# Optimization experiments

Measured on AMD Instinct MI355X. Metric: run time of the kernel, lower is better.

Reference implementation:

```python
import jax, jax.numpy as jnp
import numpy as np

N, B, E, H = 2048, 4, 256, 8
DH = E // H


def setup_inputs() -> dict:
    key = jax.random.key(0)
    ks = jax.random.split(key, 10)
    s = 1.0 / np.sqrt(E)
    f = lambda k, sh, sc=1.0: (jax.random.normal(k, sh, jnp.float32) * sc)
    return {
        "x": f(ks[0], (N, B, E)),
        "query_pos": f(ks[1], (N, B, E), 0.1),
        "receiver_val_res": f(ks[2], (N, B, E), 0.1),
        "sender_val_res": f(ks[3], (N, B, E), 0.1),
        "Wq": f(ks[4], (E, E), s), "bq": jnp.zeros((E,), jnp.float32),
        "Wk": f(ks[5], (E, E), s), "bk": jnp.zeros((E,), jnp.float32),
        "Wr": f(ks[6], (E, E), s), "br": jnp.zeros((E,), jnp.float32),
        "Ws": f(ks[7], (E, E), s), "bs_v": jnp.zeros((E,), jnp.float32),
        "Wo": f(ks[8], (E, E), s), "bo": jnp.zeros((E,), jnp.float32),
    }


def reference(x, query_pos, receiver_val_res, sender_val_res,
              Wq, bq, Wk, bk, Wr, br, Ws, bs_v, Wo, bo):
    # wrapper: key = query = x; key_pos = query_pos (same shape); residual = x
    q_in = x + query_pos  # [N,B,E]
    scale = 1.0 / np.sqrt(DH)
    q = (q_in @ Wq + bq).reshape(N, B, H, DH)
    k = (q_in @ Wk + bk).reshape(N, B, H, DH)
    # TIE edge-value decomposition: per-particle receiver/sender value tokens,
    # with accumulated cross-layer value residuals added.
    vr = q_in @ Wr + br + receiver_val_res  # [N,B,E]
    vs = q_in @ Ws + bs_v + sender_val_res  # [N,B,E]
    scores = jnp.einsum('nbhd,mbhd->bhnm', q, k) * scale  # [B,H,N,N]
    attn = jax.nn.softmax(scores, axis=-1)
    # out_i = sum_j a_ij (vr_i + vs_j) = vr_i + sum_j a_ij vs_j  (rows sum to 1)
    ctx = jnp.einsum('bhnm,mbhd->nbhd', attn, vs.reshape(N, B, H, DH))
    ctx = ctx + vr.reshape(N, B, H, DH)
    out = ctx.reshape(N, B, E) @ Wo + bo
    return (x + out, vr, vs)
```

## Files before the change

### kernel.cpp

```cpp
#include <hip/hip_runtime.h>
#include <hip/hip_bf16.h>

#define NTOK 2048
#define BATCH 4
#define EMB 256
#define NH 8
#define DHD 32
#define MROWS (NTOK*BATCH)
#define NBE (MROWS*EMB)

typedef __attribute__((ext_vector_type(8))) __bf16 bf16x8;
typedef __attribute__((ext_vector_type(4))) float f32x4;
typedef __attribute__((ext_vector_type(8))) unsigned short ushort8;
typedef __attribute__((ext_vector_type(4))) unsigned int uint4v;

__device__ __forceinline__ unsigned short f2bf(float f){
  unsigned int u = __builtin_bit_cast(unsigned int, f);
  u += 0x7fffu + ((u >> 16) & 1u);
  return (unsigned short)(u >> 16);
}
__device__ __forceinline__ float fexp2(float x){
#if __has_builtin(__builtin_amdgcn_exp2f)
  return __builtin_amdgcn_exp2f(x);
#else
  return exp2f(x);
#endif
}

#define QSC (0.17677669529663687f * 1.4426950408889634f)


__global__ __launch_bounds__(256) void k_add(const float* __restrict__ x,
                                             const float* __restrict__ qp,
                                             unsigned short* __restrict__ qpk){
  int t = blockIdx.x * 256 + threadIdx.x;
  int ppos = t * 8;
  int tile = ppos >> 12;
  int rem  = ppos & 4095;
  int kc   = rem >> 9;
  int row  = (rem >> 5) & 15;
  int kk   = rem & 31;
  int src  = (tile*16 + row)*256 + kc*32 + kk;
  f32x4 a0 = *(const f32x4*)(x + src);
  f32x4 a1 = *(const f32x4*)(x + src + 4);
  f32x4 b0 = *(const f32x4*)(qp + src);
  f32x4 b1 = *(const f32x4*)(qp + src + 4);
  ushort8 o;
#pragma unroll
  for (int j = 0; j < 4; ++j){
    o[j]   = f2bf(a0[j] + b0[j]);
    o[j+4] = f2bf(a1[j] + b1[j]);
  }
  *(ushort8*)(qpk + ppos) = o;
}

__global__ __launch_bounds__(256) void k_transW(const float* __restrict__ s0,
                                                const float* __restrict__ s1,
                                                const float* __restrict__ s2,
                                                const float* __restrict__ s3,
                                                const float* __restrict__ s4,
                                                unsigned short* __restrict__ wt){
  const float* srcs[5] = {s0, s1, s2, s3, s4};
  __shared__ float lds[64][65];
  int wi = blockIdx.z;
  int k0 = blockIdx.x * 64;
  int n0 = blockIdx.y * 64;
  int tid = threadIdx.x;
  const float* src = srcs[wi];
#pragma unroll
  for (int p = 0; p < 4; ++p){
    int r = p*16 + (tid>>4);
    int c = (tid&15)*4;
    f32x4 v = *(const f32x4*)(src + (k0+r)*256 + n0 + c);
#pragma unroll
    for (int j = 0; j < 4; ++j) lds[r][c+j] = v[j];
  }
  __syncthreads();
#pragma unroll
  for (int p = 0; p < 4; ++p){
    int nr = p*16 + (tid>>4);
    int kc = (tid&15)*4;
    unsigned long long pk = 0;
#pragma unroll
    for (int j = 0; j < 4; ++j)
      pk |= ((unsigned long long)f2bf(lds[kc+j][nr])) << (16*j);
    int n_g = n0 + nr, k_g = k0 + kc;
    int pos = (n_g>>4)*4096 + (k_g>>5)*512 + (n_g&15)*32 + (k_g&31);
    *(unsigned long long*)(wt + wi*65536 + pos) = pk;
  }
}

__global__ __launch_bounds__(256) void k_proj(const unsigned short* __restrict__ qpk,
                                              const unsigned short* __restrict__ wt,
                                              const float* __restrict__ bq,
                                              const float* __restrict__ bk,
                                              const float* __restrict__ br,
                                              const float* __restrict__ bs,
                                              const float* __restrict__ recv,
                                              const float* __restrict__ send,
                                              unsigned short* __restrict__ qbuf,
                                              unsigned short* __restrict__ kpk,
                                              unsigned short* __restrict__ vpk,
                                              float* __restrict__ vrout,
                                              float* __restrict__ vsout){
  int m0 = blockIdx.x * 64;
  int gc = blockIdx.y * 64;
  int widx = gc >> 8;
  int c0 = gc & 255;
  int tid = threadIdx.x;
  int w = tid >> 6, lane = tid & 63;
  int lr = lane & 15, lg = lane >> 4;

  __shared__ __align__(16) float shmemF[64*68];

  const unsigned short* apk = qpk + (m0/16 + w)*4096 + lr*32 + lg*8;
  const unsigned short* bpk = wt + widx*65536 + (c0/16)*4096 + lr*32 + lg*8;

  f32x4 acc[4];
#pragma unroll
  for (int f = 0; f < 4; ++f) acc[f] = (f32x4){0.f, 0.f, 0.f, 0.f};

#pragma unroll
  for (int k0 = 0; k0 < 256; k0 += 32){
    int kb = (k0 >> 5) * 512;
    bf16x8 af = *(const bf16x8*)(apk + kb);
#pragma unroll
    for (int f = 0; f < 4; ++f){
      bf16x8 bfrag = *(const bf16x8*)(bpk + f*4096 + kb);
      acc[f] = __builtin_amdgcn_mfma_f32_16x16x32_bf16(af, bfrag, acc[f], 0, 0, 0);
    }
  }

  const float* bias = (widx == 0) ? bq : (widx == 1) ? bk : (widx == 2) ? br : bs;

  if (widx <= 1){
    unsigned short (*st)[16][72] = (unsigned short(*)[16][72])shmemF;
#pragma unroll
    for (int f = 0; f < 4; ++f){
#pragma unroll
      for (int i = 0; i < 4; ++i){
        int c = c0 + f*16 + lr;
        float v = acc[f][i] + bias[c];
        st[w][lg*4+i][f*16+lr] = f2bf(widx == 0 ? v * QSC : v);
      }
    }
    if (widx == 0){
      int r = lane >> 2, co = (lane & 3) * 16;
      ushort8 a0 = *(ushort8*)&st[w][r][co];
      ushort8 a1 = *(ushort8*)&st[w][r][co + 8];
      unsigned short* dst = qbuf + (m0 + w*16 + r) * 256 + c0 + co;
      *(ushort8*)dst = a0;
      *(ushort8*)(dst + 8) = a1;
    } else {
      int cid = lane >> 3, s = lane & 7;
      int bb = cid >> 1, hr = cid & 1;
      int toko = s >> 1, dp = (s & 1) * 16;
      ushort8 a0 = *(ushort8*)&st[w][toko*4 + bb][hr*32 + dp];
      ushort8 a1 = *(ushort8*)&st[w][toko*4 + bb][hr*32 + dp + 8];
      int h  = (c0 >> 5) + hr;
      int n0 = (m0 + w*16) >> 2;
      int t0 = n0 & 63;
      int p0 = (((t0>>5)&1)<<4) + (((t0>>2)&1)<<5) + (((t0>>3)&3)<<2);
      unsigned short* dst = kpk + (bb*8 + h)*65536 + ((n0 & ~63) + p0 + toko)*32 + dp;
      *(ushort8*)dst = a0;
      *(ushort8*)(dst + 8) = a1;
    }
  } else {
    float (*ldsF)[68] = (float(*)[68])shmemF;
#pragma unroll
    for (int f = 0; f < 4; ++f){
#pragma unroll
      for (int i = 0; i < 4; ++i){
        ldsF[w*16 + lg*4 + i][f*16 + lr] = acc[f][i] + bias[c0 + f*16 + lr];
      }
    }
    __syncthreads();
    const float* gsrc = (widx == 2) ? recv : send;
    float* gdst = (widx == 2) ? vrout : vsout;
#pragma unroll
    for (int k = 0; k < 4; ++k){
      int chunk = k*256 + tid;
      int r = chunk >> 4;
      int cc = (chunk & 15) * 4;
      int idx = (m0 + r)*256 + c0 + cc;
      f32x4 v = *(const f32x4*)&ldsF[r][cc];
      f32x4 g = *(const f32x4*)(gsrc + idx);
#pragma unroll
      for (int j = 0; j < 4; ++j) v[j] += g[j];
      *(f32x4*)(gdst + idx) = v;
    }
    if (widx == 3){
      int bid = blockIdx.x;
      int tile = bid >> 1;
      int cid = tid >> 5;
      int bb = cid >> 1, hr = cid & 1;
      int d = tid & 31;
      int h0 = c0 >> 5;
      int bh = bb*8 + h0 + hr;
      unsigned short* tbase = vpk + (bh*64 + tile)*1024 + d*8;
#pragma unroll
      for (int s8 = 0; s8 < 2; ++s8){
        int sub = 2*(bid & 1) + s8;
        ushort8 o;
#pragma unroll
        for (int j = 0; j < 8; ++j)
          o[j] = f2bf(ldsF[(s8*8 + j)*4 + bb][hr*32 + d] + gsrc[(m0 + (s8*8+j)*4 + bb)*256 + c0 + hr*32 + d]);
        *(ushort8*)(tbase + sub*256) = o;
      }
    }
  }
}

__global__ __launch_bounds__(256) void k_attn(const unsigned short* __restrict__ qbuf,
                                              const unsigned short* __restrict__ kpk,
                                              const unsigned short* __restrict__ vpk,
                                              const float* __restrict__ vrbuf,
                                              unsigned short* __restrict__ ctx){
  int bid = blockIdx.x;
  int bh  = (bid & 7) + ((bid >> 8) << 3);
  int qt0 = ((bid >> 3) & 31) * 64;
  int b = bh >> 3, h = bh & 7;
  int tid = threadIdx.x;
  int w = tid >> 6, lane = tid & 63;
  int wq = w & 1;
  int wk = w >> 1;
  int lr = lane & 15, lg = lane >> 4;
  int lg4 = lg * 4;

  __shared__ float part[2][2][64][9];

  int qbase = qt0 + wq*32;
  bf16x8 qfA = *(const bf16x8*)(qbuf + ((qbase + lr)*BATCH + b)*EMB + h*DHD + lg*8);
  bf16x8 qfB = *(const bf16x8*)(qbuf + ((qbase + 16 + lr)*BATCH + b)*EMB + h*DHD + lg*8);

  const unsigned short* kbase = kpk + bh*65536 + wk*(1024*32) + lr*32 + lg*8;
  const unsigned short* vbase = vpk + bh*65536 + wk*(32*1024) + lg*256 + lr*8;

  f32x4 accA0 = (f32x4){0.f,0.f,0.f,0.f};
  f32x4 accA1 = (f32x4){0.f,0.f,0.f,0.f};
  f32x4 accB0 = (f32x4){0.f,0.f,0.f,0.f};
  f32x4 accB1 = (f32x4){0.f,0.f,0.f,0.f};
  float lsumA = 0.f, lsumB = 0.f;

  bf16x8 kA[4], vA[4], kB[4], vB[4];

  auto loadfr = [&](int kv0, bf16x8* kf, bf16x8* vf){
#pragma unroll
    for (int j = 0; j < 4; ++j)
      kf[j] = *(const bf16x8*)(kbase + (kv0 + j*16)*32);
#pragma unroll
    for (int c = 0; c < 2; ++c)
#pragma unroll
      for (int dh = 0; dh < 2; ++dh)
        vf[c*2+dh] = *(const bf16x8*)(vbase + ((kv0>>5) + c)*1024 + dh*128);
  };

  auto tile_compute = [&](const bf16x8* kf, const bf16x8* vf){
    f32x4 z = (f32x4){0.f,0.f,0.f,0.f};
    f32x4 sA[4], sB[4];
#pragma unroll
    for (int j = 0; j < 4; ++j){
      sA[j] = __builtin_amdgcn_mfma_f32_16x16x32_bf16(kf[j], qfA, z, 0, 0, 0);
      sB[j] = __builtin_amdgcn_mfma_f32_16x16x32_bf16(kf[j], qfB, z, 0, 0, 0);
    }

    float pA[4][4], pB[4][4];
    float psA = 0.f, psB = 0.f;
#pragma unroll
    for (int j = 0; j < 4; ++j){
#pragma unroll
      for (int i = 0; i < 4; ++i){
        pA[j][i] = fexp2(sA[j][i]);
        pB[j][i] = fexp2(sB[j][i]);
      }
      psA += (pA[j][0] + pA[j][1]) + (pA[j][2] + pA[j][3]);
      psB += (pB[j][0] + pB[j][1]) + (pB[j][2] + pB[j][3]);
    }
    lsumA += psA;
    lsumB += psB;

#pragma unroll
    for (int c = 0; c < 2; ++c){
      uint4v dA, dB;
      dA[0] = __builtin_amdgcn_perm(__builtin_bit_cast(unsigned int, pA[c][1]),
                                    __builtin_bit_cast(unsigned int, pA[c][0]), 0x07060302u);
      dA[1] = __builtin_amdgcn_perm(__builtin_bit_cast(unsigned int, pA[c][3]),
                                    __builtin_bit_cast(unsigned int, pA[c][2]), 0x07060302u);
      dA[2] = __builtin_amdgcn_perm(__builtin_bit_cast(unsigned int, pA[c+2][1]),
                                    __builtin_bit_cast(unsigned int, pA[c+2][0]), 0x07060302u);
      dA[3] = __builtin_amdgcn_perm(__builtin_bit_cast(unsigned int, pA[c+2][3]),
                                    __builtin_bit_cast(unsigned int, pA[c+2][2]), 0x07060302u);
      bf16x8 pfA = __builtin_bit_cast(bf16x8, dA);
      accA0 = __builtin_amdgcn_mfma_f32_16x16x32_bf16(pfA, vf[c*2+0], accA0, 0, 0, 0);
      accA1 = __builtin_amdgcn_mfma_f32_16x16x32_bf16(pfA, vf[c*2+1], accA1, 0, 0, 0);
      dB[0] = __builtin_amdgcn_perm(__builtin_bit_cast(unsigned int, pB[c][1]),
                                    __builtin_bit_cast(unsigned int, pB[c][0]), 0x07060302u);
      dB[1] = __builtin_amdgcn_perm(__builtin_bit_cast(unsigned int, pB[c][3]),
                                    __builtin_bit_cast(unsigned int, pB[c][2]), 0x07060302u);
      dB[2] = __builtin_amdgcn_perm(__builtin_bit_cast(unsigned int, pB[c+2][1]),
                                    __builtin_bit_cast(unsigned int, pB[c+2][0]), 0x07060302u);
      dB[3] = __builtin_amdgcn_perm(__builtin_bit_cast(unsigned int, pB[c+2][3]),
                                    __builtin_bit_cast(unsigned int, pB[c+2][2]), 0x07060302u);
      bf16x8 pfB = __builtin_bit_cast(bf16x8, dB);
      accB0 = __builtin_amdgcn_mfma_f32_16x16x32_bf16(pfB, vf[c*2+0], accB0, 0, 0, 0);
      accB1 = __builtin_amdgcn_mfma_f32_16x16x32_bf16(pfB, vf[c*2+1], accB1, 0, 0, 0);
    }
  };

  loadfr(0, kA, vA);
  for (int t = 0; t < 16; t += 2){
    loadfr((t+1)*64, kB, vB);
    tile_compute(kA, vA);
    if (t + 2 < 16) loadfr((t+2)*64, kA, vA);
    tile_compute(kB, vB);
  }

  lsumA += __shfl_xor(lsumA, 16);
  lsumA += __shfl_xor(lsumA, 32);
  lsumB += __shfl_xor(lsumB, 16);
  lsumB += __shfl_xor(lsumB, 32);

  if (wk == 1){
#pragma unroll
    for (int i = 0; i < 4; ++i){
      part[wq][0][lane][i]   = accA0[i];
      part[wq][0][lane][4+i] = accA1[i];
      part[wq][1][lane][i]   = accB0[i];
      part[wq][1][lane][4+i] = accB1[i];
    }
    part[wq][0][lane][8] = lsumA;
    part[wq][1][lane][8] = lsumB;
  }
  __syncthreads();
  if (wk == 0){
#pragma unroll
    for (int i = 0; i < 4; ++i){
      accA0[i] += part[wq][0][lane][i];
      accA1[i] += part[wq][0][lane][4+i];
      accB0[i] += part[wq][1][lane][i];
      accB1[i] += part[wq][1][lane][4+i];
    }
    lsumA += part[wq][0][lane][8];
    lsumB += part[wq][1][lane][8];
    float invA = 1.0f / lsumA;
    float invB = 1.0f / lsumB;
#pragma unroll
    for (int i = 0; i < 4; ++i){
      float vinvA = __shfl(invA, lg4 + i);
      float vinvB = __shfl(invB, lg4 + i);
      int qA = qbase + lg4 + i;
      int idxA = (qA*4 + b)*256 + h*DHD + lr;
      int posA = (qA>>2)*4096 + h*512 + (4*(qA&3)+b)*32 + lr;
      ctx[posA]      = f2bf(accA0[i] * vinvA + vrbuf[idxA]);
      ctx[posA + 16] = f2bf(accA1[i] * vinvA + vrbuf[idxA + 16]);
      int qB = qbase + 16 + lg4 + i;
      int idxB = (qB*4 + b)*256 + h*DHD + lr;
      int posB = (qB>>2)*4096 + h*512 + (4*(qB&3)+b)*32 + lr;
      ctx[posB]      = f2bf(accB0[i] * vinvB + vrbuf[idxB]);
      ctx[posB + 16] = f2bf(accB1[i] * vinvB + vrbuf[idxB + 16]);
    }
  }
}

__global__ __launch_bounds__(256) void k_out(const unsigned short* __restrict__ ctx,
                                             const unsigned short* __restrict__ wt,
                                             const float* __restrict__ bo,
                                             const float* __restrict__ x,
                                             float* __restrict__ out0){
  int m0 = blockIdx.x * 64;
  int c0 = blockIdx.y * 64;
  int tid = threadIdx.x;
  int w = tid >> 6, lane = tid & 63;
  int lr = lane & 15, lg = lane >> 4;

  __shared__ __align__(16) float ldsF[64][68];

  const unsigned short* apk = ctx + (m0/16 + w)*4096 + lr*32 + lg*8;
  const unsigned short* bpk = wt + 4*65536 + (c0/16)*4096 + lr*32 + lg*8;

  f32x4 acc[4];
#pragma unroll
  for (int f = 0; f < 4; ++f) acc[f] = (f32x4){0.f, 0.f, 0.f, 0.f};

#pragma unroll
  for (int k0 = 0; k0 < 256; k0 += 32){
    int kb = (k0 >> 5) * 512;
    bf16x8 af = *(const bf16x8*)(apk + kb);
#pragma unroll
    for (int f = 0; f < 4; ++f){
      bf16x8 bfrag = *(const bf16x8*)(bpk + f*4096 + kb);
      acc[f] = __builtin_amdgcn_mfma_f32_16x16x32_bf16(af, bfrag, acc[f], 0, 0, 0);
    }
  }

#pragma unroll
  for (int f = 0; f < 4; ++f){
#pragma unroll
    for (int i = 0; i < 4; ++i){
      ldsF[w*16 + lg*4 + i][f*16 + lr] = acc[f][i] + bo[c0 + f*16 + lr];
    }
  }
  __syncthreads();
#pragma unroll
  for (int k = 0; k < 4; ++k){
    int chunk = k*256 + tid;
    int r = chunk >> 4;
    int cc = (chunk & 15) * 4;
    int idx = (m0 + r)*256 + c0 + cc;
    f32x4 v = *(const f32x4*)&ldsF[r][cc];
    f32x4 g = *(const f32x4*)(x + idx);
#pragma unroll
    for (int j = 0; j < 4; ++j) v[j] += g[j];
    *(f32x4*)(out0 + idx) = v;
  }
}

extern "C" void kernel_launch(void* const* d_in, const int* in_sizes, int n_in,
                              void* d_out, int out_size, void* d_ws, size_t ws_size,
                              hipStream_t stream){
  const float* x    = (const float*)d_in[0];
  const float* qp   = (const float*)d_in[1];
  const float* recv = (const float*)d_in[2];
  const float* send = (const float*)d_in[3];
  const float* Wq   = (const float*)d_in[4];
  const float* bq   = (const float*)d_in[5];
  const float* Wk   = (const float*)d_in[6];
  const float* bk   = (const float*)d_in[7];
  const float* Wr   = (const float*)d_in[8];
  const float* br   = (const float*)d_in[9];
  const float* Wsv  = (const float*)d_in[10];
  const float* bsv  = (const float*)d_in[11];
  const float* Wo   = (const float*)d_in[12];
  const float* bo   = (const float*)d_in[13];

  float* out0  = (float*)d_out;
  float* vrout = out0 + NBE;
  float* vsout = out0 + 2*NBE;

  unsigned short* ws   = (unsigned short*)d_ws;
  unsigned short* qin  = ws;
  unsigned short* qbuf = ws + NBE;
  unsigned short* kpk  = ws + 2*NBE;
  unsigned short* vpk  = ws + 3*NBE;
  unsigned short* wt   = ws + 4*NBE;

  hipLaunchKernelGGL(k_add, dim3(NBE/8/256), dim3(256), 0, stream, x, qp, qin);
  hipLaunchKernelGGL(k_transW, dim3(4, 4, 5), dim3(256), 0, stream, Wq, Wk, Wr, Wsv, Wo, wt);
  hipLaunchKernelGGL(k_proj, dim3(128, 16), dim3(256), 0, stream,
                     qin, wt, bq, bk, br, bsv, recv, send, qbuf, kpk, vpk, vrout, vsout);
  hipLaunchKernelGGL(k_attn, dim3(1024), dim3(256), 0, stream,
                     qbuf, kpk, vpk, vrout, qin );
  hipLaunchKernelGGL(k_out, dim3(128, 4), dim3(256), 0, stream,
                     qin , wt, bo, x, out0);
}
```

Measured before the change: 78.84 us.

## Split attention KV range across four waves per 32-query block

Each attention block now handles 32 queries instead of 64, and its four waves each cover a quarter of the key/value sequence rather than two waves per half. The grid doubles to 2048 blocks, and partial accumulators from three waves are reduced through shared memory into wave 0. Launch bounds now request higher occupancy (6 blocks per CU). The aim is more parallelism and a shorter serial KV loop per wave. The cost is that K/V traffic per query is duplicated across more blocks and the shared-memory reduction gets larger.

```diff
diff --git a/kernel.cpp b/kernel.cpp
--- a/kernel.cpp
+++ b/kernel.cpp
@@ -211,30 +211,27 @@
   }
 }
 
-__global__ __launch_bounds__(256) void k_attn(const unsigned short* __restrict__ qbuf,
-                                              const unsigned short* __restrict__ kpk,
-                                              const unsigned short* __restrict__ vpk,
-                                              const float* __restrict__ vrbuf,
-                                              unsigned short* __restrict__ ctx){
+__global__ __launch_bounds__(256, 6) void k_attn(const unsigned short* __restrict__ qbuf,
+                                                 const unsigned short* __restrict__ kpk,
+                                                 const unsigned short* __restrict__ vpk,
+                                                 const float* __restrict__ vrbuf,
+                                                 unsigned short* __restrict__ ctx){
   int bid = blockIdx.x;
-  int bh  = (bid & 7) + ((bid >> 8) << 3);
-  int qt0 = ((bid >> 3) & 31) * 64;
+  int bh  = (bid & 7) + ((bid >> 9) << 3);
+  int qbase = ((bid >> 3) & 63) * 32;
   int b = bh >> 3, h = bh & 7;
   int tid = threadIdx.x;
   int w = tid >> 6, lane = tid & 63;
-  int wq = w & 1;
-  int wk = w >> 1;
   int lr = lane & 15, lg = lane >> 4;
   int lg4 = lg * 4;
 
-  __shared__ float part[2][2][64][9];
-
-  int qbase = qt0 + wq*32;
+  __shared__ float part[3][2][64][9];
+
   bf16x8 qfA = *(const bf16x8*)(qbuf + ((qbase + lr)*BATCH + b)*EMB + h*DHD + lg*8);
   bf16x8 qfB = *(const bf16x8*)(qbuf + ((qbase + 16 + lr)*BATCH + b)*EMB + h*DHD + lg*8);
 
-  const unsigned short* kbase = kpk + bh*65536 + wk*(1024*32) + lr*32 + lg*8;
-  const unsigned short* vbase = vpk + bh*65536 + wk*(32*1024) + lg*256 + lr*8;
+  const unsigned short* kbase = kpk + bh*65536 + w*16384 + lr*32 + lg*8;
+  const unsigned short* vbase = vpk + bh*65536 + w*16384 + lg*256 + lr*8;
 
   f32x4 accA0 = (f32x4){0.f,0.f,0.f,0.f};
   f32x4 accA1 = (f32x4){0.f,0.f,0.f,0.f};
@@ -308,10 +305,10 @@
   };
 
   loadfr(0, kA, vA);
-  for (int t = 0; t < 16; t += 2){
+  for (int t = 0; t < 8; t += 2){
     loadfr((t+1)*64, kB, vB);
     tile_compute(kA, vA);
-    if (t + 2 < 16) loadfr((t+2)*64, kA, vA);
+    if (t + 2 < 8) loadfr((t+2)*64, kA, vA);
     tile_compute(kB, vB);
   }
 
@@ -320,28 +317,31 @@
   lsumB += __shfl_xor(lsumB, 16);
   lsumB += __shfl_xor(lsumB, 32);
 
-  if (wk == 1){
+  if (w > 0){
 #pragma unroll
     for (int i = 0; i < 4; ++i){
-      part[wq][0][lane][i]   = accA0[i];
-      part[wq][0][lane][4+i] = accA1[i];
-      part[wq][1][lane][i]   = accB0[i];
-      part[wq][1][lane][4+i] = accB1[i];
-    }
-    part[wq][0][lane][8] = lsumA;
-    part[wq][1][lane][8] = lsumB;
+      part[w-1][0][lane][i]   = accA0[i];
+      part[w-1][0][lane][4+i] = accA1[i];
+      part[w-1][1][lane][i]   = accB0[i];
+      part[w-1][1][lane][4+i] = accB1[i];
+    }
+    part[w-1][0][lane][8] = lsumA;
+    part[w-1][1][lane][8] = lsumB;
   }
   __syncthreads();
-  if (wk == 0){
-#pragma unroll
-    for (int i = 0; i < 4; ++i){
-      accA0[i] += part[wq][0][lane][i];
-      accA1[i] += part[wq][0][lane][4+i];
-      accB0[i] += part[wq][1][lane][i];
-      accB1[i] += part[wq][1][lane][4+i];
-    }
-    lsumA += part[wq][0][lane][8];
-    lsumB += part[wq][1][lane][8];
+  if (w == 0){
+#pragma unroll
+    for (int ww = 0; ww < 3; ++ww){
+#pragma unroll
+      for (int i = 0; i < 4; ++i){
+        accA0[i] += part[ww][0][lane][i];
+        accA1[i] += part[ww][0][lane][4+i];
+        accB0[i] += part[ww][1][lane][i];
+        accB1[i] += part[ww][1][lane][4+i];
+      }
+      lsumA += part[ww][0][lane][8];
+      lsumB += part[ww][1][lane][8];
+    }
     float invA = 1.0f / lsumA;
     float invB = 1.0f / lsumB;
 #pragma unroll
@@ -448,7 +448,7 @@
   hipLaunchKernelGGL(k_transW, dim3(4, 4, 5), dim3(256), 0, stream, Wq, Wk, Wr, Wsv, Wo, wt);
   hipLaunchKernelGGL(k_proj, dim3(128, 16), dim3(256), 0, stream,
                      qin, wt, bq, bk, br, bsv, recv, send, qbuf, kpk, vpk, vrout, vsout);
-  hipLaunchKernelGGL(k_attn, dim3(1024), dim3(256), 0, stream,
+  hipLaunchKernelGGL(k_attn, dim3(2048), dim3(256), 0, stream,
                      qbuf, kpk, vpk, vrout, qin );
   hipLaunchKernelGGL(k_out, dim3(128, 4), dim3(256), 0, stream,
                      qin , wt, bo, x, out0);
```

Result: slower. 211.6 us (+168.5%).
